# Performance work log

Hardware: AMD Instinct MI355X
Metric: run time of the kernel (lower is better)

## Reference

```python
import jax, jax.numpy as jnp
import numpy as np

B, S, D = 8, 1024, 1024
H, DH = 16, 64
FF = 4096
EPS = 1e-5


def setup_inputs() -> dict:
    key = jax.random.key(0)
    ks = jax.random.split(key, 16)
    sd = 1.0 / np.sqrt(D)
    sp = 1.0 / np.sqrt(H * DH)
    sf = 1.0 / np.sqrt(FF)
    return {
        "x": jax.random.normal(ks[0], (B, S, D), jnp.float32),
        # per-head QKV projections stacked: [H, D, DH]
        "wq": jax.random.uniform(ks[1], (H, D, DH), jnp.float32, -sd, sd),
        "bq": jax.random.uniform(ks[2], (H, DH), jnp.float32, -sd, sd),
        "wk": jax.random.uniform(ks[3], (H, D, DH), jnp.float32, -sd, sd),
        "bk": jax.random.uniform(ks[4], (H, DH), jnp.float32, -sd, sd),
        "wv": jax.random.uniform(ks[5], (H, D, DH), jnp.float32, -sd, sd),
        "bv": jax.random.uniform(ks[6], (H, DH), jnp.float32, -sd, sd),
        "wo": jax.random.uniform(ks[7], (H * DH, D), jnp.float32, -sp, sp),
        "bo": jax.random.uniform(ks[8], (D,), jnp.float32, -sp, sp),
        "w1": jax.random.uniform(ks[9], (D, FF), jnp.float32, -sd, sd),
        "b1": jax.random.uniform(ks[10], (FF,), jnp.float32, -sd, sd),
        "w2": jax.random.uniform(ks[11], (FF, D), jnp.float32, -sf, sf),
        "b2": jax.random.uniform(ks[12], (D,), jnp.float32, -sf, sf),
        "g1": jnp.ones((D,), jnp.float32),
        "be1": jnp.zeros((D,), jnp.float32),
        "g2": jnp.ones((D,), jnp.float32),
        "be2": jnp.zeros((D,), jnp.float32),
    }


def _layernorm(x, g, b):
    mu = jnp.mean(x, axis=-1, keepdims=True)
    var = jnp.mean((x - mu) ** 2, axis=-1, keepdims=True)
    return (x - mu) * jax.lax.rsqrt(var + EPS) * g + b


def reference(x, wq, bq, wk, bk, wv, bv, wo, bo, w1, b1, w2, b2, g1, be1, g2, be2):
    # batched multi-head attention (math identical to the per-head torch loop)
    q = jnp.einsum('bsd,hde->bhse', x, wq) + bq[None, :, None, :]
    k = jnp.einsum('bsd,hde->bhse', x, wk) + bk[None, :, None, :]
    v = jnp.einsum('bsd,hde->bhse', x, wv) + bv[None, :, None, :]
    scores = jnp.einsum('bhse,bhte->bhst', q, k) / jnp.sqrt(jnp.float32(DH))
    probs = jax.nn.softmax(scores, axis=-1)
    ctx = jnp.einsum('bhst,bhte->bhse', probs, v)  # [B,H,S,DH]
    ctx = ctx.transpose(0, 2, 1, 3).reshape(B, S, H * DH)  # concat over heads
    attn = ctx @ wo + bo
    # dropout is identity in eval mode
    x = _layernorm(x + attn, g1, be1)
    ffn = jax.nn.relu(x @ w1 + b1) @ w2 + b2
    x = _layernorm(x + ffn, g2, be2)
    return x
```

## Files before the change

### kernel.cpp

```cpp
#include <hip/hip_runtime.h>
#include <hip/hip_bf16.h>

#define Bb 8
#define Ss 1024
#define Dd 1024
#define Hh 16
#define DHh 64
#define FFf 4096

typedef __hip_bfloat16 bf16;
typedef __attribute__((ext_vector_type(8))) __bf16 bf16x8;
typedef __attribute__((ext_vector_type(4))) float f32x4;

__device__ __forceinline__ unsigned short f2bu(float f) {
  __hip_bfloat16 h = __float2bfloat16(f);
  return __builtin_bit_cast(unsigned short, h);
}

#define MFMA16(a, b, c) __builtin_amdgcn_mfma_f32_16x16x32_bf16((a), (b), (c), 0, 0, 0)

__device__ __forceinline__ void gl_lds16(const void* g, void* l) {
  __builtin_amdgcn_global_load_lds(
      (const __attribute__((address_space(1))) unsigned int*)g,
      (__attribute__((address_space(3))) unsigned int*)l, 16, 0, 0);
}

__global__ __launch_bounds__(256) void f32_to_bf16_vec(const float* __restrict__ in,
                                                       bf16* __restrict__ out, int n4) {
  int i = blockIdx.x * 256 + threadIdx.x;
  if (i < n4) {
    float4 v = ((const float4*)in)[i];
    union { unsigned short u[4]; uint2 q; } r;
    r.u[0] = f2bu(v.x); r.u[1] = f2bu(v.y); r.u[2] = f2bu(v.z); r.u[3] = f2bu(v.w);
    ((uint2*)out)[i] = r.q;
  }
}

__global__ __launch_bounds__(256) void transpose_f32_bf16(const float* __restrict__ src,
                                                          bf16* __restrict__ dst,
                                                          int R, int C,
                                                          long sbatch, long dbatch) {
  __shared__ float tile[32][33];
  src += (size_t)blockIdx.z * sbatch;
  dst += (size_t)blockIdx.z * dbatch;
  int c0 = blockIdx.x * 32, r0 = blockIdx.y * 32;
  int tx = threadIdx.x & 31;
  int ty = threadIdx.x >> 5;
#pragma unroll
  for (int kk = 0; kk < 4; ++kk)
    tile[ty + kk * 8][tx] = src[(size_t)(r0 + ty + kk * 8) * C + c0 + tx];
  __syncthreads();
#pragma unroll
  for (int kk = 0; kk < 4; ++kk)
    dst[(size_t)(c0 + ty + kk * 8) * R + r0 + tx] = __float2bfloat16(tile[tx][ty + kk * 8]);
}

enum { EPI_QKV = 0, EPI_WO = 1, EPI_FFN1 = 2, EPI_FFN2 = 3 };

__device__ __forceinline__ void stage_u(const bf16* __restrict__ G, int ldK,
                                        int row0, int kt, int u,
                                        unsigned char* ldsbase, int tid) {
  const int r = u * 32 + (tid >> 3);
  const int seg = (tid & 7) ^ (r & 7);
  gl_lds16(G + (size_t)(row0 + r) * ldK + kt + seg * 8,
           ldsbase + u * 4096 + (tid >> 6) * 1024);
}

template <int EPI>
__global__ __launch_bounds__(256) void gemm_bt(const bf16* __restrict__ A,
                                               const bf16* __restrict__ Bt,
                                               int M, int N, int K,
                                               const float* __restrict__ bias0,
                                               const float* __restrict__ bias1,
                                               const float* __restrict__ bias2,
                                               void* __restrict__ o0,
                                               void* __restrict__ o1,
                                               void* __restrict__ o2) {
  __shared__ __align__(16) unsigned char sm[32768];
  const int t = threadIdx.x;
  const int lane = t & 63;
  const int w = t >> 6;
  const int wr = w >> 1;
  const int wc = w & 1;
  const int m0 = blockIdx.x * 128;
  const int n0 = blockIdx.y * 128;
  const int rl = lane & 15, ks = lane >> 4;

  f32x4 acc[4][4];
  const f32x4 z4 = {0.f, 0.f, 0.f, 0.f};
#pragma unroll
  for (int i = 0; i < 4; ++i)
#pragma unroll
    for (int j = 0; j < 4; ++j) acc[i][j] = z4;

  for (int kt = 0; kt < K; kt += 64) {
    __syncthreads();
#pragma unroll
    for (int u = 0; u < 4; ++u) stage_u(A, K, m0, kt, u, sm, t);
#pragma unroll
    for (int u = 0; u < 4; ++u) stage_u(Bt, K, n0, kt, u, sm + 16384, t);
    __syncthreads();

    bf16x8 a[4][2], b[4][2];
#pragma unroll
    for (int i = 0; i < 4; ++i) {
#pragma unroll
      for (int kk = 0; kk < 2; ++kk) {
        const int row = wr * 64 + i * 16 + rl;
        a[i][kk] = *(const bf16x8*)(sm + row * 128 + (((kk * 4 + ks) ^ (row & 7)) << 4));
        const int col = wc * 64 + i * 16 + rl;
        b[i][kk] = *(const bf16x8*)(sm + 16384 + col * 128 + (((kk * 4 + ks) ^ (col & 7)) << 4));
      }
    }
#pragma unroll
    for (int i = 0; i < 4; ++i)
#pragma unroll
      for (int j = 0; j < 4; ++j)
#pragma unroll
        for (int kk = 0; kk < 2; ++kk)
          acc[i][j] = MFMA16(a[i][kk], b[j][kk], acc[i][j]);
  }

  const int rbase = ks * 4;
  if constexpr (EPI == EPI_QKV) {
    const int which = n0 >> 10;
    const float* bias = which == 0 ? bias0 : (which == 1 ? bias1 : bias2);
    bf16* dst = (bf16*)(which == 0 ? o0 : (which == 1 ? o1 : o2));
#pragma unroll
    for (int i = 0; i < 4; ++i) {
#pragma unroll
      for (int j = 0; j < 4; ++j) {
        const int gcol = n0 + wc * 64 + j * 16 + rl;
        const int cc = gcol & 1023;
        const int hh = cc >> 6, e = cc & 63;
        const float bval = bias[cc];
#pragma unroll
        for (int p = 0; p < 4; ++p) {
          const int grow = m0 + wr * 64 + i * 16 + rbase + p;
          const int bidx = grow >> 10, s = grow & 1023;
          if (which == 2) {
            dst[(((size_t)bidx * Hh + hh) * DHh + e) * Ss + s] =
                __float2bfloat16(acc[i][j][p] + bval);
          } else {
            dst[(((size_t)bidx * Hh + hh) * Ss + s) * DHh + e] =
                __float2bfloat16(acc[i][j][p] + bval);
          }
        }
      }
    }
  } else if constexpr (EPI == EPI_WO || EPI == EPI_FFN2) {
    float* dst = (float*)o0;
#pragma unroll
    for (int i = 0; i < 4; ++i) {
#pragma unroll
      for (int j = 0; j < 4; ++j) {
        const int gcol = n0 + wc * 64 + j * 16 + rl;
        const float bval = bias0[gcol];
#pragma unroll
        for (int p = 0; p < 4; ++p) {
          const int grow = m0 + wr * 64 + i * 16 + rbase + p;
          dst[(size_t)grow * N + gcol] = acc[i][j][p] + bval;
        }
      }
    }
  } else {
    bf16* dst = (bf16*)o0;
#pragma unroll
    for (int i = 0; i < 4; ++i) {
#pragma unroll
      for (int j = 0; j < 4; ++j) {
        const int gcol = n0 + wc * 64 + j * 16 + rl;
        const float bval = bias0[gcol];
#pragma unroll
        for (int p = 0; p < 4; ++p) {
          const int grow = m0 + wr * 64 + i * 16 + rbase + p;
          dst[(size_t)grow * N + gcol] =
              __float2bfloat16(fmaxf(acc[i][j][p] + bval, 0.f));
        }
      }
    }
  }
}

__global__ __launch_bounds__(256) void attn_kernel(const bf16* __restrict__ q,
                                                   const bf16* __restrict__ k,
                                                   const bf16* __restrict__ v,
                                                   bf16* __restrict__ ctx) {
  __shared__ __align__(16) unsigned short Kl[64 * 64];
  __shared__ __align__(16) unsigned short Vt[64 * 64];
  __shared__ __align__(16) unsigned short Pl[4 * 16 * 72];

  const int bid = blockIdx.x;
  const int xcd = bid & 7;
  const int s8 = bid >> 3;
  const int hg = xcd + 8 * (s8 >> 4);
  const int qi = s8 & 15;
  const int b = hg >> 4, h = hg & 15;
  const int q0 = qi * 64;
  const size_t head = (size_t)hg << 16;
  const bf16* Qp = q + head;
  const bf16* Kp = k + head;
  const bf16* Vp = v + head;

  const int t = threadIdx.x;
  const int w = t >> 6;
  const int lane = t & 63;
  const int rl = lane & 15;
  const int ks = lane >> 4;
  const int rx = rl & 7;

  const int qrow = q0 + w * 16 + rl;
  const bf16x8 aq0 = *(const bf16x8*)(Qp + (size_t)qrow * 64 + ks * 8);
  const bf16x8 aq1 = *(const bf16x8*)(Qp + (size_t)qrow * 64 + 32 + ks * 8);

  f32x4 o[4];
  const f32x4 z4 = {0.f, 0.f, 0.f, 0.f};
#pragma unroll
  for (int c = 0; c < 4; ++c) o[c] = z4;
  float m4[4] = {-1e30f, -1e30f, -1e30f, -1e30f};
  float l4[4] = {0.f, 0.f, 0.f, 0.f};

  const int rt = t >> 2;
  const int st = t & 3;
  const int wof0 = rt * 64 + ((st ^ (rt & 7)) << 3);
  const int wof1 = rt * 64 + (((st + 4) ^ (rt & 7)) << 3);
  unsigned short* Pw = Pl + w * 16 * 72;
  const float scale = 0.125f;

  bf16x8 kr0 = *(const bf16x8*)(Kp + (size_t)rt * 64 + st * 8);
  bf16x8 kr1 = *(const bf16x8*)(Kp + (size_t)rt * 64 + (st + 4) * 8);
  bf16x8 vr0 = *(const bf16x8*)(Vp + (size_t)rt * Ss + st * 8);
  bf16x8 vr1 = *(const bf16x8*)(Vp + (size_t)rt * Ss + (st + 4) * 8);

  for (int kv0 = 0; kv0 < Ss; kv0 += 64) {
    __syncthreads();
    *(bf16x8*)(Kl + wof0) = kr0;
    *(bf16x8*)(Kl + wof1) = kr1;
    *(bf16x8*)(Vt + wof0) = vr0;
    *(bf16x8*)(Vt + wof1) = vr1;
    if (kv0 + 64 < Ss) {
      kr0 = *(const bf16x8*)(Kp + (size_t)(kv0 + 64 + rt) * 64 + st * 8);
      kr1 = *(const bf16x8*)(Kp + (size_t)(kv0 + 64 + rt) * 64 + (st + 4) * 8);
      vr0 = *(const bf16x8*)(Vp + (size_t)rt * Ss + kv0 + 64 + st * 8);
      vr1 = *(const bf16x8*)(Vp + (size_t)rt * Ss + kv0 + 64 + (st + 4) * 8);
    }
    __syncthreads();

    f32x4 s4[4];
#pragma unroll
    for (int f = 0; f < 4; ++f) s4[f] = z4;
#pragma unroll
    for (int f = 0; f < 4; ++f) {
      const int row = f * 16 + rl;
      const bf16x8 b0 = *(const bf16x8*)(Kl + row * 64 + (ks ^ rx) * 8);
      const bf16x8 b1 = *(const bf16x8*)(Kl + row * 64 + ((4 + ks) ^ rx) * 8);
      s4[f] = MFMA16(aq0, b0, s4[f]);
      s4[f] = MFMA16(aq1, b1, s4[f]);
    }

    float mx[4], sm[4];
#pragma unroll
    for (int j = 0; j < 4; ++j) {
      s4[0][j] *= scale; s4[1][j] *= scale; s4[2][j] *= scale; s4[3][j] *= scale;
      mx[j] = fmaxf(fmaxf(s4[0][j], s4[1][j]), fmaxf(s4[2][j], s4[3][j]));
    }
#pragma unroll
    for (int mm = 1; mm < 16; mm <<= 1)
#pragma unroll
      for (int j = 0; j < 4; ++j) mx[j] = fmaxf(mx[j], __shfl_xor(mx[j], mm, 64));
#pragma unroll
    for (int j = 0; j < 4; ++j) {
      const float mn = fmaxf(m4[j], mx[j]);
      const float corr = __expf(m4[j] - mn);
      m4[j] = mn;
#pragma unroll
      for (int f = 0; f < 4; ++f) s4[f][j] = __expf(s4[f][j] - mn);
      sm[j] = (s4[0][j] + s4[1][j]) + (s4[2][j] + s4[3][j]);
      l4[j] *= corr;
#pragma unroll
      for (int c = 0; c < 4; ++c) o[c][j] *= corr;
    }
#pragma unroll
    for (int mm = 1; mm < 16; mm <<= 1)
#pragma unroll
      for (int j = 0; j < 4; ++j) sm[j] += __shfl_xor(sm[j], mm, 64);
#pragma unroll
    for (int j = 0; j < 4; ++j) l4[j] += sm[j];

#pragma unroll
    for (int f = 0; f < 4; ++f)
#pragma unroll
      for (int j = 0; j < 4; ++j)
        Pw[(ks * 4 + j) * 72 + f * 16 + rl] = f2bu(s4[f][j]);
    asm volatile("s_waitcnt lgkmcnt(0)" ::: "memory");
    __builtin_amdgcn_sched_barrier(0);
    const bf16x8 pa0 = *(const bf16x8*)(Pw + rl * 72 + ks * 8);
    const bf16x8 pa1 = *(const bf16x8*)(Pw + rl * 72 + 32 + ks * 8);

#pragma unroll
    for (int c = 0; c < 4; ++c) {
      const int row = c * 16 + rl;
      const bf16x8 v0 = *(const bf16x8*)(Vt + row * 64 + (ks ^ rx) * 8);
      const bf16x8 v1 = *(const bf16x8*)(Vt + row * 64 + ((4 + ks) ^ rx) * 8);
      o[c] = MFMA16(pa0, v0, o[c]);
      o[c] = MFMA16(pa1, v1, o[c]);
    }
  }

  float inv[4];
#pragma unroll
  for (int j = 0; j < 4; ++j) inv[j] = 1.0f / l4[j];
#pragma unroll
  for (int c = 0; c < 4; ++c) {
#pragma unroll
    for (int j = 0; j < 4; ++j) {
      const int sq = q0 + w * 16 + ks * 4 + j;
      const int dh = c * 16 + rl;
      ctx[(((size_t)b * Ss + sq) * Hh + h) * DHh + dh] =
          __float2bfloat16(o[c][j] * inv[j]);
    }
  }
}

__global__ __launch_bounds__(256) void ln_fused(const float* __restrict__ a,
                                                const float* __restrict__ bsrc,
                                                const float* __restrict__ g,
                                                const float* __restrict__ be,
                                                float* __restrict__ of,
                                                bf16* __restrict__ ob) {
  const int row = blockIdx.x, t = threadIdx.x;
  const float4 va = ((const float4*)(a + (size_t)row * Dd))[t];
  const float4 vb = ((const float4*)(bsrc + (size_t)row * Dd))[t];
  const float x0 = va.x + vb.x, x1 = va.y + vb.y, x2 = va.z + vb.z, x3 = va.w + vb.w;
  float s = x0 + x1 + x2 + x3;
  float qq = x0 * x0 + x1 * x1 + x2 * x2 + x3 * x3;
#pragma unroll
  for (int m = 1; m < 64; m <<= 1) {
    s += __shfl_xor(s, m, 64);
    qq += __shfl_xor(qq, m, 64);
  }
  __shared__ float ss[4], sq2[4];
  if ((t & 63) == 0) {
    ss[t >> 6] = s;
    sq2[t >> 6] = qq;
  }
  __syncthreads();
  s = ss[0] + ss[1] + ss[2] + ss[3];
  qq = sq2[0] + sq2[1] + sq2[2] + sq2[3];
  const float mu = s * (1.0f / Dd);
  const float var = qq * (1.0f / Dd) - mu * mu;
  const float rs = rsqrtf(var + 1e-5f);
  const float4 gv = ((const float4*)g)[t];
  const float4 bv = ((const float4*)be)[t];
  const float y0 = (x0 - mu) * rs * gv.x + bv.x;
  const float y1 = (x1 - mu) * rs * gv.y + bv.y;
  const float y2 = (x2 - mu) * rs * gv.z + bv.z;
  const float y3 = (x3 - mu) * rs * gv.w + bv.w;
  if (of) ((float4*)(of + (size_t)row * Dd))[t] = make_float4(y0, y1, y2, y3);
  if (ob) {
    union { unsigned short u[4]; uint2 qv; } r;
    r.u[0] = f2bu(y0); r.u[1] = f2bu(y1); r.u[2] = f2bu(y2); r.u[3] = f2bu(y3);
    ((uint2*)(ob + (size_t)row * Dd))[t] = r.qv;
  }
}

extern "C" void kernel_launch(void* const* d_in, const int* in_sizes, int n_in,
                              void* d_out, int out_size, void* d_ws, size_t ws_size,
                              hipStream_t stream) {
  const float* x   = (const float*)d_in[0];
  const float* wq  = (const float*)d_in[1];
  const float* bq  = (const float*)d_in[2];
  const float* wk  = (const float*)d_in[3];
  const float* bk  = (const float*)d_in[4];
  const float* wv  = (const float*)d_in[5];
  const float* bv  = (const float*)d_in[6];
  const float* wo  = (const float*)d_in[7];
  const float* bo  = (const float*)d_in[8];
  const float* w1  = (const float*)d_in[9];
  const float* b1  = (const float*)d_in[10];
  const float* w2  = (const float*)d_in[11];
  const float* b2  = (const float*)d_in[12];
  const float* g1  = (const float*)d_in[13];
  const float* be1 = (const float*)d_in[14];
  const float* g2  = (const float*)d_in[15];
  const float* be2 = (const float*)d_in[16];
  float* out = (float*)d_out;

  char* ws = (char*)d_ws;
  const size_t MB = 1u << 20;
  bf16* qb    = (bf16*)(ws + 0);
  bf16* kb    = (bf16*)(ws + 16 * MB);
  bf16* vvb   = (bf16*)(ws + 32 * MB);
  bf16* xb    = (bf16*)(ws + 48 * MB);
  bf16* hb    = (bf16*)(ws + 0);
  bf16* ctx   = (bf16*)(ws + 64 * MB);
  float* y    = (float*)(ws + 80 * MB);
  float* x1f  = (float*)(ws + 112 * MB);
  bf16* x1b   = (bf16*)(ws + 144 * MB);
  bf16* btqkv = (bf16*)(ws + 160 * MB);
  bf16* wot   = (bf16*)(ws + 166 * MB);
  bf16* w1t   = (bf16*)(ws + 168 * MB);
  bf16* w2t   = (bf16*)(ws + 176 * MB);

  f32_to_bf16_vec<<<8192, 256, 0, stream>>>(x, xb, Bb * Ss * Dd / 4);
  transpose_f32_bf16<<<dim3(2, 32, 16), 256, 0, stream>>>(wq, btqkv + 0 * 1048576,
                                                          Dd, DHh, 65536, 65536);
  transpose_f32_bf16<<<dim3(2, 32, 16), 256, 0, stream>>>(wk, btqkv + 1 * 1048576,
                                                          Dd, DHh, 65536, 65536);
  transpose_f32_bf16<<<dim3(2, 32, 16), 256, 0, stream>>>(wv, btqkv + 2 * 1048576,
                                                          Dd, DHh, 65536, 65536);
  transpose_f32_bf16<<<dim3(32, 32, 1), 256, 0, stream>>>(wo, wot, Hh * DHh, Dd, 0, 0);
  transpose_f32_bf16<<<dim3(128, 32, 1), 256, 0, stream>>>(w1, w1t, Dd, FFf, 0, 0);
  transpose_f32_bf16<<<dim3(32, 128, 1), 256, 0, stream>>>(w2, w2t, FFf, Dd, 0, 0);

  gemm_bt<EPI_QKV><<<dim3(64, 24), 256, 0, stream>>>(
      xb, btqkv, Bb * Ss, 3 * Hh * DHh, Dd, bq, bk, bv, qb, kb, vvb);

  attn_kernel<<<2048, 256, 0, stream>>>(qb, kb, vvb, ctx);

  gemm_bt<EPI_WO><<<dim3(64, 8), 256, 0, stream>>>(
      ctx, wot, Bb * Ss, Dd, Hh * DHh, bo, nullptr, nullptr, y, nullptr, nullptr);

  ln_fused<<<Bb * Ss, 256, 0, stream>>>(x, y, g1, be1, x1f, x1b);

  gemm_bt<EPI_FFN1><<<dim3(64, 32), 256, 0, stream>>>(
      x1b, w1t, Bb * Ss, FFf, Dd, b1, nullptr, nullptr, hb, nullptr, nullptr);
  gemm_bt<EPI_FFN2><<<dim3(64, 8), 256, 0, stream>>>(
      hb, w2t, Bb * Ss, Dd, FFf, b2, nullptr, nullptr, y, nullptr, nullptr);

  ln_fused<<<Bb * Ss, 256, 0, stream>>>(x1f, y, g2, be2, out, nullptr);
}
```

Baseline: 560.8 us.

## Widen attention KV tile to 128, load via global_load_lds, lazy softmax rescale

The attention kernel now processes 128 keys per iteration instead of 64, staging K and V tiles straight into LDS with global_load_lds (XOR-swizzled addresses) in place of register prefetch followed by LDS stores. The online softmax skips the rescale of the running max, sum and output unless some row's max grows by more than 8, and the scale is folded into the exponent. This cuts barriers and loop overhead per key and removes register staging, but it drops the register prefetch that overlapped the next tile's global load with compute, raises LDS use, and lets exp values reach up to e^8 before normalisation.

```diff
diff --git a/kernel.cpp b/kernel.cpp
--- a/kernel.cpp
+++ b/kernel.cpp
@@ -186,9 +186,9 @@
                                                    const bf16* __restrict__ k,
                                                    const bf16* __restrict__ v,
                                                    bf16* __restrict__ ctx) {
-  __shared__ __align__(16) unsigned short Kl[64 * 64];
-  __shared__ __align__(16) unsigned short Vt[64 * 64];
-  __shared__ __align__(16) unsigned short Pl[4 * 16 * 72];
+  __shared__ __align__(16) unsigned short Kl[128 * 64];
+  __shared__ __align__(16) unsigned short Vt[64 * 128];
+  __shared__ __align__(16) unsigned short Pl[4 * 16 * 136];
 
   const int bid = blockIdx.x;
   const int xcd = bid & 7;
@@ -207,7 +207,6 @@
   const int lane = t & 63;
   const int rl = lane & 15;
   const int ks = lane >> 4;
-  const int rx = rl & 7;
 
   const int qrow = q0 + w * 16 + rl;
   const bf16x8 aq0 = *(const bf16x8*)(Qp + (size_t)qrow * 64 + ks * 8);
@@ -220,40 +219,36 @@
   float m4[4] = {-1e30f, -1e30f, -1e30f, -1e30f};
   float l4[4] = {0.f, 0.f, 0.f, 0.f};
 
-  const int rt = t >> 2;
-  const int st = t & 3;
-  const int wof0 = rt * 64 + ((st ^ (rt & 7)) << 3);
-  const int wof1 = rt * 64 + (((st + 4) ^ (rt & 7)) << 3);
-  unsigned short* Pw = Pl + w * 16 * 72;
+  unsigned short* Pw = Pl + w * 16 * 136;
   const float scale = 0.125f;
 
-  bf16x8 kr0 = *(const bf16x8*)(Kp + (size_t)rt * 64 + st * 8);
-  bf16x8 kr1 = *(const bf16x8*)(Kp + (size_t)rt * 64 + (st + 4) * 8);
-  bf16x8 vr0 = *(const bf16x8*)(Vp + (size_t)rt * Ss + st * 8);
-  bf16x8 vr1 = *(const bf16x8*)(Vp + (size_t)rt * Ss + (st + 4) * 8);
-
-  for (int kv0 = 0; kv0 < Ss; kv0 += 64) {
+  const int kr8 = lane >> 3, ksg = lane & 7;
+  const int vr4 = lane >> 4, vsg = lane & 15;
+
+  for (int kv0 = 0; kv0 < Ss; kv0 += 128) {
     __syncthreads();
-    *(bf16x8*)(Kl + wof0) = kr0;
-    *(bf16x8*)(Kl + wof1) = kr1;
-    *(bf16x8*)(Vt + wof0) = vr0;
-    *(bf16x8*)(Vt + wof1) = vr1;
-    if (kv0 + 64 < Ss) {
-      kr0 = *(const bf16x8*)(Kp + (size_t)(kv0 + 64 + rt) * 64 + st * 8);
-      kr1 = *(const bf16x8*)(Kp + (size_t)(kv0 + 64 + rt) * 64 + (st + 4) * 8);
-      vr0 = *(const bf16x8*)(Vp + (size_t)rt * Ss + kv0 + 64 + st * 8);
-      vr1 = *(const bf16x8*)(Vp + (size_t)rt * Ss + kv0 + 64 + (st + 4) * 8);
+#pragma unroll
+    for (int u = 0; u < 4; ++u) {
+      const int row = u * 32 + w * 8 + kr8;
+      gl_lds16(Kp + (size_t)(kv0 + row) * 64 + (ksg ^ (row & 7)) * 8,
+               Kl + u * 2048 + w * 512);
+    }
+#pragma unroll
+    for (int u = 0; u < 4; ++u) {
+      const int d = u * 16 + w * 4 + vr4;
+      gl_lds16(Vp + (size_t)d * Ss + kv0 + ((vsg ^ (d & 7)) * 8),
+               Vt + u * 2048 + w * 512);
     }
     __syncthreads();
 
-    f32x4 s4[4];
-#pragma unroll
-    for (int f = 0; f < 4; ++f) s4[f] = z4;
-#pragma unroll
-    for (int f = 0; f < 4; ++f) {
+    f32x4 s4[8];
+#pragma unroll
+    for (int f = 0; f < 8; ++f) s4[f] = z4;
+#pragma unroll
+    for (int f = 0; f < 8; ++f) {
       const int row = f * 16 + rl;
-      const bf16x8 b0 = *(const bf16x8*)(Kl + row * 64 + (ks ^ rx) * 8);
-      const bf16x8 b1 = *(const bf16x8*)(Kl + row * 64 + ((4 + ks) ^ rx) * 8);
+      const bf16x8 b0 = *(const bf16x8*)(Kl + row * 64 + ((ks ^ (row & 7)) * 8));
+      const bf16x8 b1 = *(const bf16x8*)(Kl + row * 64 + (((4 + ks) ^ (row & 7)) * 8));
       s4[f] = MFMA16(aq0, b0, s4[f]);
       s4[f] = MFMA16(aq1, b1, s4[f]);
     }
@@ -261,24 +256,33 @@
     float mx[4], sm[4];
 #pragma unroll
     for (int j = 0; j < 4; ++j) {
-      s4[0][j] *= scale; s4[1][j] *= scale; s4[2][j] *= scale; s4[3][j] *= scale;
-      mx[j] = fmaxf(fmaxf(s4[0][j], s4[1][j]), fmaxf(s4[2][j], s4[3][j]));
+      float m01 = fmaxf(s4[0][j], s4[1][j]), m23 = fmaxf(s4[2][j], s4[3][j]);
+      float m45 = fmaxf(s4[4][j], s4[5][j]), m67 = fmaxf(s4[6][j], s4[7][j]);
+      mx[j] = fmaxf(fmaxf(m01, m23), fmaxf(m45, m67)) * scale;
     }
 #pragma unroll
     for (int mm = 1; mm < 16; mm <<= 1)
 #pragma unroll
       for (int j = 0; j < 4; ++j) mx[j] = fmaxf(mx[j], __shfl_xor(mx[j], mm, 64));
+    const int nogrow = (mx[0] <= m4[0] + 8.f) && (mx[1] <= m4[1] + 8.f) &&
+                       (mx[2] <= m4[2] + 8.f) && (mx[3] <= m4[3] + 8.f);
+    if (!__all(nogrow)) {
+#pragma unroll
+      for (int j = 0; j < 4; ++j) {
+        const float mn = fmaxf(m4[j], mx[j]);
+        const float corr = __expf(m4[j] - mn);
+        m4[j] = mn;
+        l4[j] *= corr;
+#pragma unroll
+        for (int c = 0; c < 4; ++c) o[c][j] *= corr;
+      }
+    }
 #pragma unroll
     for (int j = 0; j < 4; ++j) {
-      const float mn = fmaxf(m4[j], mx[j]);
-      const float corr = __expf(m4[j] - mn);
-      m4[j] = mn;
-#pragma unroll
-      for (int f = 0; f < 4; ++f) s4[f][j] = __expf(s4[f][j] - mn);
-      sm[j] = (s4[0][j] + s4[1][j]) + (s4[2][j] + s4[3][j]);
-      l4[j] *= corr;
-#pragma unroll
-      for (int c = 0; c < 4; ++c) o[c][j] *= corr;
+#pragma unroll
+      for (int f = 0; f < 8; ++f) s4[f][j] = __expf(s4[f][j] * scale - m4[j]);
+      sm[j] = ((s4[0][j] + s4[1][j]) + (s4[2][j] + s4[3][j])) +
+              ((s4[4][j] + s4[5][j]) + (s4[6][j] + s4[7][j]));
     }
 #pragma unroll
     for (int mm = 1; mm < 16; mm <<= 1)
@@ -288,22 +292,25 @@
     for (int j = 0; j < 4; ++j) l4[j] += sm[j];
 
 #pragma unroll
-    for (int f = 0; f < 4; ++f)
+    for (int f = 0; f < 8; ++f)
 #pragma unroll
       for (int j = 0; j < 4; ++j)
-        Pw[(ks * 4 + j) * 72 + f * 16 + rl] = f2bu(s4[f][j]);
+        Pw[(ks * 4 + j) * 136 + f * 16 + rl] = f2bu(s4[f][j]);
     asm volatile("s_waitcnt lgkmcnt(0)" ::: "memory");
     __builtin_amdgcn_sched_barrier(0);
-    const bf16x8 pa0 = *(const bf16x8*)(Pw + rl * 72 + ks * 8);
-    const bf16x8 pa1 = *(const bf16x8*)(Pw + rl * 72 + 32 + ks * 8);
+    bf16x8 pa[4];
+#pragma unroll
+    for (int cc = 0; cc < 4; ++cc)
+      pa[cc] = *(const bf16x8*)(Pw + rl * 136 + cc * 32 + ks * 8);
 
 #pragma unroll
     for (int c = 0; c < 4; ++c) {
-      const int row = c * 16 + rl;
-      const bf16x8 v0 = *(const bf16x8*)(Vt + row * 64 + (ks ^ rx) * 8);
-      const bf16x8 v1 = *(const bf16x8*)(Vt + row * 64 + ((4 + ks) ^ rx) * 8);
-      o[c] = MFMA16(pa0, v0, o[c]);
-      o[c] = MFMA16(pa1, v1, o[c]);
+      const int d = c * 16 + rl;
+#pragma unroll
+      for (int cc = 0; cc < 4; ++cc) {
+        const bf16x8 vb = *(const bf16x8*)(Vt + d * 128 + (((cc * 4 + ks) ^ (d & 7)) * 8));
+        o[c] = MFMA16(pa[cc], vb, o[c]);
+      }
     }
   }
 
```

Result: faster. 533.5 us (-4.9%).
